# Kernel optimization log

Hardware: AMD Instinct MI355X
Metric: run time of the kernel (lower is better)

Reference implementation:

```python
import jax, jax.numpy as jnp
import numpy as np

TANH_SCALAR = 10.0  # taug in IrEne eq. 1 (close_to_one setting)

N_NODES = 2**21 - 1   # complete binary tree, depth D=21
N_LEAVES = 2**20
NUM_FEATURES = 64


def setup_inputs() -> dict:
    key = jax.random.key(0)
    k1, k2, k3, k4 = jax.random.split(key, 4)
    features = jax.random.normal(k1, (N_NODES, NUM_FEATURES), dtype=jnp.float32)
    leaf_energy = jax.random.uniform(k2, (N_LEAVES,), dtype=jnp.float32)
    W = jax.random.normal(k3, (NUM_FEATURES, 1), dtype=jnp.float32) * 0.1
    b = jax.random.normal(k4, (1,), dtype=jnp.float32) * 0.1
    return {"features": features, "leaf_energy": leaf_energy, "W": W, "b": b}


def reference(features, leaf_energy, W, b):
    """Batched equivalent of RecursiveTreeComputation (close_to_one, end2end).

    Tree layout: complete binary tree in level order; node i's parent is (i-1)//2.
    Level d occupies indices [2^d - 1, 2^{d+1} - 1). Leaves are the last level.
    parent_energy = sum_children score(child) * child_energy,
    score(f) = 1 + tanh(f @ W + b) / tanh_scalar.
    Returns predicted energy for every node, shape [N].
    """
    N, F = features.shape
    D = int(np.log2(N + 1))  # number of levels (static)

    # One fused pass over all nodes: Linear(F,1) + tanh + affine (WeightingModel).
    scores = 1.0 + jnp.tanh(features @ W + b)[:, 0] / TANH_SCALAR  # [N]

    leaf_start = 2 ** (D - 1) - 1
    energy = jnp.zeros((N,), dtype=features.dtype).at[leaf_start:].set(leaf_energy)

    # Level-wise bottom-up accumulation; consecutive child pairs share a parent.
    for d in range(D - 1, 0, -1):
        start, end = 2 ** d - 1, 2 ** (d + 1) - 1          # children at level d
        contrib = scores[start:end] * energy[start:end]      # weighted child energies
        parent_vals = contrib.reshape(-1, 2).sum(axis=1)     # sum sibling pairs
        pstart = 2 ** (d - 1) - 1                             # parents at level d-1
        energy = energy.at[pstart:start].set(energy[pstart:start] + parent_vals)
    return energy
```

## Files before the change

kernel.cpp:

```cpp
#include <hip/hip_runtime.h>
#include <cmath>

#define N_NODES_C   ((1 << 21) - 1)
#define N_LEAVES_C  (1 << 20)
#define LEAF_START  (N_LEAVES_C - 1)
#define NFEAT       64

__device__ __forceinline__ float score_fn(float dot, float bias) {
    return 1.0f + tanhf(dot + bias) * 0.1f;
}

__device__ __forceinline__ float dot16(const float4 f, const float4 w) {
    float v = f.x * w.x + f.y * w.y + f.z * w.z + f.w * w.w;
    v += __shfl_xor(v, 1);
    v += __shfl_xor(v, 2);
    v += __shfl_xor(v, 4);
    v += __shfl_xor(v, 8);
    return v;
}

__global__ __launch_bounds__(256) void tree_reduce_kernel(
        const float* __restrict__ features,
        const float* __restrict__ leaf_energy,
        const float* __restrict__ W,
        const float* __restrict__ b,
        float* __restrict__ out) {
    __shared__ float sc[512];
    __shared__ float buf[2][512];
    const int tid = threadIdx.x;
    const int q   = tid & 15;
    const int grp = tid >> 4;
    const int blk = blockIdx.x;
    const float4 w4 = ((const float4*)W)[q];
    const float bias = b[0];
    const int l0 = blk << 9;

    for (int i = tid; i < 512; i += 256)
        out[LEAF_START + l0 + i] = leaf_energy[l0 + i];

    for (int pd = 19; pd >= 12; --pd) {
        const int m = 1 << (pd - 11);
        const int gbase = ((1 << pd) - 1) + blk * m;
        const int off = 512 - 2 * m;
        for (int j = grp; j < m; j += 16) {
            const float4 f = ((const float4*)(features + (size_t)(gbase + j) * NFEAT))[q];
            const float v = dot16(f, w4);
            if (q == 0) sc[off + j] = score_fn(v, bias);
        }
    }

    for (int j = grp; j < 512; j += 16) {
        const size_t g = (size_t)(LEAF_START + l0 + j);
        const float4 f = ((const float4*)(features + g * NFEAT))[q];
        const float v = dot16(f, w4);
        if (q == 0) buf[0][j] = score_fn(v, bias) * leaf_energy[l0 + j];
    }

    int p = 0;
    for (int pd = 19; pd >= 11; --pd) {
        const int m = 1 << (pd - 11);
        __syncthreads();
        const int gbase = ((1 << pd) - 1) + blk * m;
        for (int j = tid; j < m; j += 256) {
            const float val = buf[p][2 * j] + buf[p][2 * j + 1];
            out[gbase + j] = val;
            if (pd > 11)
                buf[1 - p][j] = sc[(512 - 2 * m) + j] * val;
        }
        p ^= 1;
    }
}

__global__ __launch_bounds__(1024) void top_kernel(
        const float* __restrict__ features,
        const float* __restrict__ W,
        const float* __restrict__ b,
        float* __restrict__ out) {
    __shared__ float slds[4096];
    __shared__ float buf[2][2048];
    const int tid = threadIdx.x;
    const int q   = tid & 15;
    const int grp = tid >> 4;
    const float4 w4 = ((const float4*)W)[q];
    const float bias = b[0];

    for (int j = grp; j < 4095; j += 64) {
        const float4 f = ((const float4*)(features + (size_t)j * NFEAT))[q];
        const float v = dot16(f, w4);
        if (q == 0) slds[j] = score_fn(v, bias);
    }
    __syncthreads();

    for (int i = tid; i < 2048; i += 1024)
        buf[0][i] = slds[2047 + i] * out[2047 + i];

    int p = 0;
    for (int pd = 10; pd >= 0; --pd) {
        const int m = 1 << pd;
        __syncthreads();
        const int base = m - 1;
        for (int j = tid; j < m; j += 1024) {
            const float val = buf[p][2 * j] + buf[p][2 * j + 1];
            out[base + j] = val;
            if (pd > 0)
                buf[1 - p][j] = slds[base + j] * val;
        }
        p ^= 1;
    }
}

extern "C" void kernel_launch(void* const* d_in, const int* in_sizes, int n_in,
                              void* d_out, int out_size, void* d_ws, size_t ws_size,
                              hipStream_t stream) {
    (void)in_sizes; (void)n_in; (void)out_size; (void)d_ws; (void)ws_size;
    const float* features    = (const float*)d_in[0];
    const float* leaf_energy = (const float*)d_in[1];
    const float* W           = (const float*)d_in[2];
    const float* b           = (const float*)d_in[3];
    float* out = (float*)d_out;

    tree_reduce_kernel<<<2048, 256, 0, stream>>>(features, leaf_energy, W, b, out);
    top_kernel<<<1, 1024, 0, stream>>>(features, W, b, out);
}
```

Before: 739.6 us.

## Split scoring into a streaming kernel and reduce the tree from a workspace

Scoring of every node moves into one grid-stride streaming kernel in which 8 lanes read a 256-byte feature row. It writes scores, or score times leaf energy for leaves, to a workspace buffer. Two small reduction kernels then walk the tree using only those scalars, so the previous kernel's poorly balanced per-block feature reads go away and the top kernel no longer reads features at all. The cost is an extra launch and an extra round trip of about 8 MB of scores through global memory.

New measurement: 701.1 us. 5.2% less time.

```diff
diff --git a/kernel.cpp b/kernel.cpp
--- a/kernel.cpp
+++ b/kernel.cpp
@@ -10,92 +10,90 @@
     return 1.0f + tanhf(dot + bias) * 0.1f;
 }
 
-__device__ __forceinline__ float dot16(const float4 f, const float4 w) {
-    float v = f.x * w.x + f.y * w.y + f.z * w.z + f.w * w.w;
-    v += __shfl_xor(v, 1);
-    v += __shfl_xor(v, 2);
-    v += __shfl_xor(v, 4);
-    v += __shfl_xor(v, 8);
-    return v;
-}
-
-__global__ __launch_bounds__(256) void tree_reduce_kernel(
+__global__ __launch_bounds__(256) void score_stream_kernel(
         const float* __restrict__ features,
         const float* __restrict__ leaf_energy,
         const float* __restrict__ W,
         const float* __restrict__ b,
+        float* __restrict__ ws,
         float* __restrict__ out) {
-    __shared__ float sc[512];
-    __shared__ float buf[2][512];
-    const int tid = threadIdx.x;
-    const int q   = tid & 15;
-    const int grp = tid >> 4;
-    const int blk = blockIdx.x;
-    const float4 w4 = ((const float4*)W)[q];
+    const int q = threadIdx.x & 7;
+    const float4 wl = ((const float4*)W)[q];
+    const float4 wh = ((const float4*)W)[q + 8];
     const float bias = b[0];
-    const int l0 = blk << 9;
-
-    for (int i = tid; i < 512; i += 256)
-        out[LEAF_START + l0 + i] = leaf_energy[l0 + i];
-
-    for (int pd = 19; pd >= 12; --pd) {
-        const int m = 1 << (pd - 11);
-        const int gbase = ((1 << pd) - 1) + blk * m;
-        const int off = 512 - 2 * m;
-        for (int j = grp; j < m; j += 16) {
-            const float4 f = ((const float4*)(features + (size_t)(gbase + j) * NFEAT))[q];
-            const float v = dot16(f, w4);
-            if (q == 0) sc[off + j] = score_fn(v, bias);
+    const int g0 = (blockIdx.x * 256 + threadIdx.x) >> 3;
+    const int gstride = (gridDim.x * 256) >> 3;
+    for (int node = g0; node < N_NODES_C; node += gstride) {
+        const float4* fp = (const float4*)(features + (size_t)node * NFEAT);
+        const float4 a = fp[q];
+        const float4 c = fp[q + 8];
+        float v = a.x * wl.x + a.y * wl.y + a.z * wl.z + a.w * wl.w
+                + c.x * wh.x + c.y * wh.y + c.z * wh.z + c.w * wh.w;
+        v += __shfl_xor(v, 1);
+        v += __shfl_xor(v, 2);
+        v += __shfl_xor(v, 4);
+        if (q == 0) {
+            const float s = score_fn(v, bias);
+            if (node >= LEAF_START) {
+                const float e = leaf_energy[node - LEAF_START];
+                ws[node] = s * e;
+                out[node] = e;
+            } else {
+                ws[node] = s;
+            }
         }
     }
+}
 
-    for (int j = grp; j < 512; j += 16) {
-        const size_t g = (size_t)(LEAF_START + l0 + j);
-        const float4 f = ((const float4*)(features + g * NFEAT))[q];
-        const float v = dot16(f, w4);
-        if (q == 0) buf[0][j] = score_fn(v, bias) * leaf_energy[l0 + j];
+__global__ __launch_bounds__(256) void mid_reduce_kernel(
+        const float* __restrict__ ws,
+        float* __restrict__ out) {
+    __shared__ float sc[1024];
+    __shared__ float buf[2][1024];
+    const int tid = threadIdx.x;
+    const int blk = blockIdx.x;
+
+    const int lbase = LEAF_START + (blk << 10);
+    for (int i = tid; i < 1024; i += 256)
+        buf[0][i] = ws[lbase + i];
+
+    for (int pd = 19; pd >= 11; --pd) {
+        const int m = 1 << (pd - 10);
+        const int gbase = ((1 << pd) - 1) + blk * m;
+        const int off = 1024 - 2 * m;
+        for (int j = tid; j < m; j += 256)
+            sc[off + j] = ws[gbase + j];
     }
 
     int p = 0;
-    for (int pd = 19; pd >= 11; --pd) {
-        const int m = 1 << (pd - 11);
+    for (int pd = 19; pd >= 10; --pd) {
+        const int m = 1 << (pd - 10);
         __syncthreads();
         const int gbase = ((1 << pd) - 1) + blk * m;
         for (int j = tid; j < m; j += 256) {
             const float val = buf[p][2 * j] + buf[p][2 * j + 1];
             out[gbase + j] = val;
-            if (pd > 11)
-                buf[1 - p][j] = sc[(512 - 2 * m) + j] * val;
+            if (pd > 10)
+                buf[1 - p][j] = sc[(1024 - 2 * m) + j] * val;
         }
         p ^= 1;
     }
 }
 
-__global__ __launch_bounds__(1024) void top_kernel(
-        const float* __restrict__ features,
-        const float* __restrict__ W,
-        const float* __restrict__ b,
+__global__ __launch_bounds__(1024) void top_reduce_kernel(
+        const float* __restrict__ ws,
         float* __restrict__ out) {
-    __shared__ float slds[4096];
-    __shared__ float buf[2][2048];
+    __shared__ float sc[2048];
+    __shared__ float buf[2][1024];
     const int tid = threadIdx.x;
-    const int q   = tid & 15;
-    const int grp = tid >> 4;
-    const float4 w4 = ((const float4*)W)[q];
-    const float bias = b[0];
-
-    for (int j = grp; j < 4095; j += 64) {
-        const float4 f = ((const float4*)(features + (size_t)j * NFEAT))[q];
-        const float v = dot16(f, w4);
-        if (q == 0) slds[j] = score_fn(v, bias);
-    }
+    for (int i = tid; i < 2047; i += 1024)
+        sc[i] = ws[i];
+    buf[0][tid] = out[1023 + tid];
     __syncthreads();
-
-    for (int i = tid; i < 2048; i += 1024)
-        buf[0][i] = slds[2047 + i] * out[2047 + i];
+    buf[0][tid] = sc[1023 + tid] * buf[0][tid];
 
     int p = 0;
-    for (int pd = 10; pd >= 0; --pd) {
+    for (int pd = 9; pd >= 0; --pd) {
         const int m = 1 << pd;
         __syncthreads();
         const int base = m - 1;
@@ -103,7 +101,7 @@
             const float val = buf[p][2 * j] + buf[p][2 * j + 1];
             out[base + j] = val;
             if (pd > 0)
-                buf[1 - p][j] = slds[base + j] * val;
+                buf[1 - p][j] = sc[base + j] * val;
         }
         p ^= 1;
     }
@@ -112,13 +110,15 @@
 extern "C" void kernel_launch(void* const* d_in, const int* in_sizes, int n_in,
                               void* d_out, int out_size, void* d_ws, size_t ws_size,
                               hipStream_t stream) {
-    (void)in_sizes; (void)n_in; (void)out_size; (void)d_ws; (void)ws_size;
+    (void)in_sizes; (void)n_in; (void)out_size; (void)ws_size;
     const float* features    = (const float*)d_in[0];
     const float* leaf_energy = (const float*)d_in[1];
     const float* W           = (const float*)d_in[2];
     const float* b           = (const float*)d_in[3];
     float* out = (float*)d_out;
+    float* ws  = (float*)d_ws;
 
-    tree_reduce_kernel<<<2048, 256, 0, stream>>>(features, leaf_energy, W, b, out);
-    top_kernel<<<1, 1024, 0, stream>>>(features, W, b, out);
+    score_stream_kernel<<<8192, 256, 0, stream>>>(features, leaf_energy, W, b, ws, out);
+    mid_reduce_kernel<<<1024, 256, 0, stream>>>(ws, out);
+    top_reduce_kernel<<<1, 1024, 0, stream>>>(ws, out);
 }
```
